# Kernel tuning notes

Measured on AMD Instinct MI355X. Metric: run time of the kernel, lower is better.

The kernel has to match this reference:

```python
import jax, jax.numpy as jnp
import numpy as np

C_IN, C = 16, 32
N = 150000
SHAPE = (480, 360, 32)
SLOPE = 0.01  # LeakyReLU default
EPS = 1e-5    # BatchNorm1d default

# offset index into the canonical 27-neighbor table, ordered (dz, dy, dx)
P133 = tuple(9 + (dy + 1) * 3 + (dx + 1) for dy in (-1, 0, 1) for dx in (-1, 0, 1))   # kernel (1,3,3)
P313 = tuple((dz + 1) * 9 + 3 + (dx + 1) for dz in (-1, 0, 1) for dx in (-1, 0, 1))   # kernel (3,1,3)
P311 = tuple((dz + 1) * 9 + 4 for dz in (-1, 0, 1))                                   # kernel (3,1,1)
P131 = tuple(9 + (dy + 1) * 3 + 1 for dy in (-1, 0, 1))                               # kernel (1,3,1)
P113 = (12, 13, 14)                                                                   # kernel (1,1,3)


def setup_inputs() -> dict:
    rng = np.random.default_rng(0)
    # unique active voxel linear coords, sorted for searchsorted lookup
    lin = np.sort(rng.choice(SHAPE[0] * SHAPE[1] * SHAPE[2], size=N, replace=False))
    z, yx = np.divmod(lin, SHAPE[1] * SHAPE[2])
    y, x = np.divmod(yx, SHAPE[2])
    coords = np.stack([z, y, x], 1)  # [N,3]
    offs = np.array([[dz, dy, dx] for dz in (-1, 0, 1) for dy in (-1, 0, 1) for dx in (-1, 0, 1)])
    nc = coords[None] + offs[:, None]  # [27,N,3]
    valid = (nc >= 0).all(-1) & (nc[..., 0] < SHAPE[0]) & (nc[..., 1] < SHAPE[1]) & (nc[..., 2] < SHAPE[2])
    nlin = nc[..., 0] * SHAPE[1] * SHAPE[2] + nc[..., 1] * SHAPE[2] + nc[..., 2]
    pos = np.clip(np.searchsorted(lin, nlin), 0, N - 1)
    found = valid & (lin[pos] == nlin)
    nbr = np.where(found, pos, -1).astype(np.int32)  # [27,N], spconv indice pairs

    key = jax.random.key(0)
    ks = jax.random.split(key, 9)
    w = lambda k, kk, ci, co: jax.random.normal(k, (kk, ci, co), jnp.float32) * (1.0 / np.sqrt(kk * ci))
    bn_params = jnp.stack([
        jnp.stack([1.0 + 0.1 * jax.random.normal(jax.random.fold_in(ks[8], 4 * i + 0), (C,)),
                   0.1 * jax.random.normal(jax.random.fold_in(ks[8], 4 * i + 1), (C,)),
                   0.1 * jax.random.normal(jax.random.fold_in(ks[8], 4 * i + 2), (C,)),
                   0.5 + jax.random.uniform(jax.random.fold_in(ks[8], 4 * i + 3), (C,))])
        for i in range(7)
    ])  # [7,4,C]: gamma, beta, running_mean, running_var
    return {
        "x_feat": jax.random.normal(ks[0], (N, C_IN), jnp.float32),
        "nbr": jnp.asarray(nbr),
        "W1": w(ks[1], 9, C_IN, C), "W12": w(ks[2], 9, C, C),
        "W2": w(ks[3], 9, C_IN, C), "W3": w(ks[4], 9, C, C),
        "Wr1": w(ks[5], 3, C, C), "Wr2": w(ks[6], 3, C, C), "Wr3": w(ks[7], 3, C, C),
        "bn_params": bn_params,
    }


def _subm(feat, nbr, W, offs):
    """Submanifold sparse conv: gather -> masked GEMM -> same active set."""
    idx = nbr[jnp.asarray(offs)]              # [K,N]
    g = feat[jnp.clip(idx, 0)]                # [K,N,Cin]
    g = jnp.where((idx >= 0)[..., None], g, jnp.zeros((), feat.dtype))
    return jnp.einsum('knc,kcd->nd', g, W)    # [N,Cout]


def _bn(f, p):  # eval-mode BatchNorm1d
    gamma, beta, mean, var = p[0], p[1], p[2], p[3]
    return gamma * (f - mean) * jax.lax.rsqrt(var + EPS) + beta


def _lrelu(f):
    return jnp.where(f >= 0, f, SLOPE * f)


def reference(x_feat, nbr, W1, W12, W2, W3, Wr1, Wr2, Wr3, bn_params):
    # ResContextBlock (downCntx): act then BN, per source
    s = _bn(_lrelu(_subm(x_feat, nbr, W1, P133)), bn_params[0])
    s = _bn(_lrelu(_subm(s, nbr, W12, P313)), bn_params[1])
    r = _bn(_lrelu(_subm(x_feat, nbr, W2, P313)), bn_params[2])
    r = _bn(_lrelu(_subm(r, nbr, W3, P133)), bn_params[3])
    y = r + s
    # ReconBlock: three axial convs -> BN -> sigmoid, summed, gating multiply
    a = jax.nn.sigmoid(_bn(_subm(y, nbr, Wr1, P311), bn_params[4]))
    b = jax.nn.sigmoid(_bn(_subm(y, nbr, Wr2, P131), bn_params[5]))
    c = jax.nn.sigmoid(_bn(_subm(y, nbr, Wr3, P113), bn_params[6]))
    return (a + b + c) * y
```

## Files before the change

### kernel.cpp

```cpp
#include <hip/hip_runtime.h>
#include <cstdint>
#include <cstddef>


#define SLOPE 0.01f
#define BN_EPS 1e-5f

typedef __attribute__((ext_vector_type(8))) short bf16x8;
typedef __attribute__((ext_vector_type(4))) float f32x4;

__device__ __forceinline__ float bflo(uint32_t w) {
    union { uint32_t i; float f; } v; v.i = w << 16; return v.f;
}
__device__ __forceinline__ float bfhi(uint32_t w) {
    union { uint32_t i; float f; } v; v.i = w & 0xffff0000u; return v.f;
}
__device__ __forceinline__ float bf2f(uint16_t u) {
    union { uint32_t i; float f; } v; v.i = ((uint32_t)u) << 16; return v.f;
}
__device__ __forceinline__ uint16_t f2bf(float f) {
    union { float f; uint32_t i; } v; v.f = f;
    uint32_t x = v.i;
    return (uint16_t)((x + 0x7fffu + ((x >> 16) & 1u)) >> 16);
}

struct Taps9 { int t[9]; };
struct WSrcs { const void* p[8]; };

#define WFS     18432
#define WF_END  (5 * WFS)
#define BN_CNT  896

__device__ __forceinline__ int detect_f32_inline(const uint16_t* x16)
{
    int lane = threadIdx.x & 63;
    float a = bf2f(x16[4 * lane]);
    float b = bf2f(x16[4 * lane + 2]);
    int bad = (!(a > -16.f && a < 16.f)) || (!(b > -16.f && b < 16.f));
    return __ballot(bad) != 0ull;
}

__device__ __forceinline__ float readw(const void* p, int j, int f32)
{
    return f32 ? ((const float*)p)[j] : bf2f(((const uint16_t*)p)[j]);
}

__global__ void prep_all(const uint16_t* __restrict__ xprobe, WSrcs srcs,
                         uint16_t* __restrict__ Wf, float* __restrict__ bnf)
{
    int f32 = detect_f32_inline(xprobe);
    int i = blockIdx.x * 256 + threadIdx.x;
    if (i < WF_END) {
        int s = i / WFS, r = i - s * WFS;
        int t = r >> 11, T = (r >> 10) & 1;
        int co = (r >> 5) & 31, k = r & 31;
        uint16_t outv;
        if (s == 0 || s == 2) {
            int c = k >> 1, p = k & 1;
            float w = readw(srcs.p[s == 0 ? 0 : 2], (t * 16 + c) * 32 + co, f32);
            uint16_t h = f2bf(w);
            outv = (T == 0) ? h : (p == 0 ? f2bf(w - bf2f(h)) : (uint16_t)0);
        } else {
            float w;
            if (s == 4) {
                int g = t / 3, kk = t - g * 3;
                const void* bnp = srcs.p[7];
                float ga = readw(bnp, (4 + g) * 128 + co, f32);
                float va = readw(bnp, (4 + g) * 128 + 96 + co, f32);
                float scl = ga * rsqrtf(va + BN_EPS);
                w = readw(srcs.p[4 + g], (kk * 32 + k) * 32 + co, f32) * scl;
            } else {
                w = readw(srcs.p[s == 1 ? 1 : 3], (t * 32 + k) * 32 + co, f32);
            }
            uint16_t h = f2bf(w);
            outv = (T == 0) ? h : f2bf(w - bf2f(h));
        }
        Wf[i] = outv;
    } else if (i < WF_END + BN_CNT) {
        bnf[i - WF_END] = readw(srcs.p[7], i - WF_END, f32);
    }
}

__global__ void canon_x3(const void* __restrict__ xsrc,
                         uint32_t* __restrict__ xi, int total)
{
    int f32 = detect_f32_inline((const uint16_t*)xsrc);
    for (int i = blockIdx.x * blockDim.x + threadIdx.x; i < total;
         i += gridDim.x * blockDim.x) {
        float v = f32 ? ((const float*)xsrc)[i]
                      : bf2f(((const uint16_t*)xsrc)[i]);
        int row = i >> 4, c = i & 15;
        uint16_t h = f2bf(v);
        uint16_t l = f2bf(v - bf2f(h));
        xi[(size_t)row * 16 + c] = (uint32_t)h | ((uint32_t)l << 16);
    }
}

struct ConvJob {
    const uint16_t* feat;
    const uint16_t* Wf;
    const float*    bn;
    const uint16_t* addsrc;
    uint16_t*       out;
    Taps9 taps;
};

#define MFMA_BF16(A, B, C) __builtin_amdgcn_mfma_f32_16x16x32_bf16(A, B, C, 0, 0, 0)

__launch_bounds__(256, 4)
__global__ void conv_mfma6(ConvJob j0, ConvJob j1,
                           const int* __restrict__ nbr, int N)
{
    const ConvJob J = (blockIdx.y == 1) ? j1 : j0;
    const int tid = threadIdx.x;
    const int n0  = blockIdx.x * 128;
    const int lane = tid & 63;
    const int m = lane & 15, q = lane >> 4;
    const int vt0 = (tid >> 6) * 32;
    const bf16x8 Z8 = {0, 0, 0, 0, 0, 0, 0, 0};

    int rows[9][2];
#pragma unroll
    for (int t = 0; t < 9; ++t)
#pragma unroll
        for (int vt = 0; vt < 2; ++vt) {
            int n = n0 + vt0 + vt * 16 + m;
            rows[t][vt] = (n < N) ? nbr[(size_t)J.taps.t[t] * N + n] : -1;
        }
    __builtin_amdgcn_sched_barrier(0);

    bool act[9][2];
#pragma unroll
    for (int t = 0; t < 9; ++t)
#pragma unroll
        for (int vt = 0; vt < 2; ++vt)
            act[t][vt] = __ballot(rows[t][vt] >= 0) != 0ull;

    f32x4 acc[2][2];
#pragma unroll
    for (int vt = 0; vt < 2; ++vt)
#pragma unroll
        for (int ot = 0; ot < 2; ++ot) acc[vt][ot] = {0.f, 0.f, 0.f, 0.f};

#pragma unroll
    for (int g = 0; g < 3; ++g) {
        bf16x8 A[3][2];
#pragma unroll
        for (int i = 0; i < 3; ++i)
#pragma unroll
            for (int vt = 0; vt < 2; ++vt) {
                const int t = g * 3 + i;
                A[i][vt] = Z8;
                if (act[t][vt]) {
                    int row = rows[t][vt];
                    if (row >= 0)
                        A[i][vt] = *(const bf16x8*)(J.feat + (size_t)row * 32 + q * 8);
                }
            }
        __builtin_amdgcn_sched_barrier(0);

#pragma unroll
        for (int i = 0; i < 3; ++i) {
            const int t = g * 3 + i;
            if (!(act[t][0] || act[t][1])) continue;
            const uint16_t* wb = J.Wf + t * 2048 + m * 32 + q * 8;
            bf16x8 B00 = *(const bf16x8*)(wb);
            bf16x8 B10 = *(const bf16x8*)(wb + 1024);
            bf16x8 B01 = *(const bf16x8*)(wb + 512);
            bf16x8 B11 = *(const bf16x8*)(wb + 1536);
#pragma unroll
            for (int vt = 0; vt < 2; ++vt) {
                if (!act[t][vt]) continue;
                acc[vt][0] = MFMA_BF16(A[i][vt], B00, acc[vt][0]);
                acc[vt][0] = MFMA_BF16(A[i][vt], B10, acc[vt][0]);
                acc[vt][1] = MFMA_BF16(A[i][vt], B01, acc[vt][1]);
                acc[vt][1] = MFMA_BF16(A[i][vt], B11, acc[vt][1]);
            }
        }
    }

#pragma unroll
    for (int ot = 0; ot < 2; ++ot) {
        int ch = ot * 16 + m;
        float ga = J.bn[ch], be = J.bn[32 + ch];
        float mu = J.bn[64 + ch], va = J.bn[96 + ch];
        float s = ga * rsqrtf(va + BN_EPS);
        float b = be - mu * s;
#pragma unroll
        for (int vt = 0; vt < 2; ++vt)
#pragma unroll
            for (int r = 0; r < 4; ++r) {
                int vox = n0 + vt0 + vt * 16 + q * 4 + r;
                if (vox >= N) continue;
                float xv = acc[vt][ot][r];
                xv = (xv >= 0.f) ? xv : SLOPE * xv;
                float o = xv * s + b;
                if (J.addsrc) o += bf2f(J.addsrc[(size_t)vox * 32 + ch]);
                J.out[(size_t)vox * 32 + ch] = f2bf(o);
            }
    }
}

__launch_bounds__(256, 4)
__global__ void recon_mfma6(const uint16_t* __restrict__ y16,
                            const uint16_t* __restrict__ xprobe,
                            const int* __restrict__ nbr,
                            const uint16_t* __restrict__ Wf4,
                            const float* __restrict__ bnf,
                            void* __restrict__ out_, int N)
{
    const int out_f32 = detect_f32_inline(xprobe);
    const int tid = threadIdx.x;
    const int n0  = blockIdx.x * 128;
    const int lane = tid & 63;
    const int m = lane & 15, q = lane >> 4;
    const int vt0 = (tid >> 6) * 32;
    const bf16x8 Z8 = {0, 0, 0, 0, 0, 0, 0, 0};

    const int ut[7] = {4, 22, 10, 16, 12, 14, 13};
    int rows[7][2];
#pragma unroll
    for (int t = 0; t < 7; ++t)
#pragma unroll
        for (int vt = 0; vt < 2; ++vt) {
            int n = n0 + vt0 + vt * 16 + m;
            rows[t][vt] = (n < N) ? nbr[(size_t)ut[t] * N + n] : -1;
        }
    __builtin_amdgcn_sched_barrier(0);

    bool act[7][2];
#pragma unroll
    for (int t = 0; t < 7; ++t)
#pragma unroll
        for (int vt = 0; vt < 2; ++vt)
            act[t][vt] = __ballot(rows[t][vt] >= 0) != 0ull;

    bf16x8 A6[2];
#pragma unroll
    for (int vt = 0; vt < 2; ++vt) {
        int row = rows[6][vt];
        A6[vt] = Z8;
        if (row >= 0)
            A6[vt] = *(const bf16x8*)(y16 + (size_t)row * 32 + q * 8);
    }

    float gsum[2][2][4];
#pragma unroll
    for (int vt = 0; vt < 2; ++vt)
#pragma unroll
        for (int ot = 0; ot < 2; ++ot)
#pragma unroll
            for (int r = 0; r < 4; ++r) gsum[vt][ot][r] = 0.f;

#pragma unroll
    for (int g = 0; g < 3; ++g) {
        f32x4 acc[2][2];
#pragma unroll
        for (int vt = 0; vt < 2; ++vt)
#pragma unroll
            for (int ot = 0; ot < 2; ++ot) acc[vt][ot] = {0.f, 0.f, 0.f, 0.f};

        bf16x8 Ae[2][2];
#pragma unroll
        for (int s2 = 0; s2 < 2; ++s2)
#pragma unroll
            for (int vt = 0; vt < 2; ++vt) {
                const int slot = 2 * g + s2;
                Ae[s2][vt] = Z8;
                if (act[slot][vt]) {
                    int row = rows[slot][vt];
                    if (row >= 0)
                        Ae[s2][vt] = *(const bf16x8*)(y16 + (size_t)row * 32 + q * 8);
                }
            }
        __builtin_amdgcn_sched_barrier(0);

#pragma unroll
        for (int s2 = 0; s2 < 2; ++s2) {
            const int slot = 2 * g + s2;
            if (!(act[slot][0] || act[slot][1])) continue;
            const int t = g * 3 + s2 * 2;
            const uint16_t* wb = Wf4 + t * 2048 + m * 32 + q * 8;
            bf16x8 B00 = *(const bf16x8*)(wb);
            bf16x8 B10 = *(const bf16x8*)(wb + 1024);
            bf16x8 B01 = *(const bf16x8*)(wb + 512);
            bf16x8 B11 = *(const bf16x8*)(wb + 1536);
#pragma unroll
            for (int vt = 0; vt < 2; ++vt) {
                if (!act[slot][vt]) continue;
                acc[vt][0] = MFMA_BF16(Ae[s2][vt], B00, acc[vt][0]);
                acc[vt][0] = MFMA_BF16(Ae[s2][vt], B10, acc[vt][0]);
                acc[vt][1] = MFMA_BF16(Ae[s2][vt], B01, acc[vt][1]);
                acc[vt][1] = MFMA_BF16(Ae[s2][vt], B11, acc[vt][1]);
            }
        }
        {
            const uint16_t* wb = Wf4 + (g * 3 + 1) * 2048 + m * 32 + q * 8;
            bf16x8 B00 = *(const bf16x8*)(wb);
            bf16x8 B10 = *(const bf16x8*)(wb + 1024);
            bf16x8 B01 = *(const bf16x8*)(wb + 512);
            bf16x8 B11 = *(const bf16x8*)(wb + 1536);
#pragma unroll
            for (int vt = 0; vt < 2; ++vt) {
                acc[vt][0] = MFMA_BF16(A6[vt], B00, acc[vt][0]);
                acc[vt][0] = MFMA_BF16(A6[vt], B10, acc[vt][0]);
                acc[vt][1] = MFMA_BF16(A6[vt], B01, acc[vt][1]);
                acc[vt][1] = MFMA_BF16(A6[vt], B11, acc[vt][1]);
            }
        }

#pragma unroll
        for (int ot = 0; ot < 2; ++ot) {
            int ch = ot * 16 + m;
            const float* p = bnf + (size_t)(4 + g) * 128;
            float scl = p[ch] * rsqrtf(p[96 + ch] + BN_EPS);
            float sh = p[32 + ch] - p[64 + ch] * scl;
#pragma unroll
            for (int vt = 0; vt < 2; ++vt)
#pragma unroll
                for (int r = 0; r < 4; ++r)
                    gsum[vt][ot][r] +=
                        1.f / (1.f + __expf(-(acc[vt][ot][r] + sh)));
        }
    }

#pragma unroll
    for (int ot = 0; ot < 2; ++ot) {
        int ch = ot * 16 + m;
#pragma unroll
        for (int vt = 0; vt < 2; ++vt)
#pragma unroll
            for (int r = 0; r < 4; ++r) {
                int vox = n0 + vt0 + vt * 16 + q * 4 + r;
                if (vox >= N) continue;
                float o = gsum[vt][ot][r] * bf2f(y16[(size_t)vox * 32 + ch]);
                if (out_f32)
                    ((float*)out_)[(size_t)vox * 32 + ch] = o;
                else
                    ((uint16_t*)out_)[(size_t)vox * 32 + ch] = f2bf(o);
            }
    }
}

#define WC_W1   0
#define WC_W12  4608
#define WC_W2   13824
#define WC_W3   18432
#define WC_WR1  27648
#define WC_WR2  30720
#define WC_WR3  33792
#define WC_BNP  36864
#define WC_END  37760

__global__ void canon_weights_fb(WSrcs srcs, float* __restrict__ Wc,
                                 const uint16_t* __restrict__ xprobe)
{
    int f32 = detect_f32_inline(xprobe);
    const int offs[9] = {WC_W1, WC_W12, WC_W2, WC_W3, WC_WR1, WC_WR2,
                         WC_WR3, WC_BNP, WC_END};
    int i = blockIdx.x * 256 + threadIdx.x;
    if (i >= WC_END) return;
    int t = 0;
#pragma unroll
    for (int k = 1; k < 8; ++k) if (i >= offs[k]) t = k;
    Wc[i] = readw(srcs.p[t], i - offs[t], f32);
}

__global__ void canon_x_bf(const void* __restrict__ xsrc,
                           uint16_t* __restrict__ xc, int n)
{
    int f32 = detect_f32_inline((const uint16_t*)xsrc);
    for (int i = blockIdx.x * blockDim.x + threadIdx.x; i < n;
         i += gridDim.x * blockDim.x) {
        float v = f32 ? ((const float*)xsrc)[i]
                      : bf2f(((const uint16_t*)xsrc)[i]);
        xc[i] = f2bf(v);
    }
}

template<int CIN>
__launch_bounds__(256)
__global__ void conv_bn_lrelu_bf(const uint16_t* __restrict__ feat,
                                 const int* __restrict__ nbr,
                                 const float* __restrict__ Wg,
                                 const float* __restrict__ bnp,
                                 const uint16_t* __restrict__ addsrc,
                                 uint16_t* __restrict__ out,
                                 Taps9 taps, int N)
{
    __shared__ float Wl[9 * CIN * 32];
    __shared__ float fs[CIN][128];
    __shared__ int   sidx[128];
    __shared__ float bns[32], bnb[32];

    const int tid = threadIdx.x;
    const int n0  = blockIdx.x * 128;

    for (int i = tid; i < 9 * CIN * 32; i += 256) Wl[i] = Wg[i];
    if (tid < 32) {
        float g = bnp[tid], b = bnp[32 + tid];
        float mu = bnp[64 + tid], va = bnp[96 + tid];
        float s = g * rsqrtf(va + BN_EPS);
        bns[tid] = s; bnb[tid] = b - mu * s;
    }
    float acc[4][4];
#pragma unroll
    for (int v = 0; v < 4; ++v)
#pragma unroll
        for (int j = 0; j < 4; ++j) acc[v][j] = 0.f;

    const int vb = (tid >> 3) << 2, cg = (tid & 7) << 2;
    const int r = tid >> 1, h = tid & 1, j0 = h * (CIN / 2);

#pragma unroll 1
    for (int t = 0; t < 9; ++t) {
        __syncthreads();
        if (tid < 128) {
            int n = n0 + tid;
            sidx[tid] = (n < N) ? nbr[(size_t)taps.t[t] * N + n] : -1;
        }
        __syncthreads();
        int mm = sidx[r];
        if (mm >= 0) {
            const uint16_t* src = feat + (size_t)mm * CIN + j0;
#pragma unroll
            for (int qq = 0; qq < CIN / 2; qq += 8) {
                uint4 u = *reinterpret_cast<const uint4*>(src + qq);
                fs[j0 + qq + 0][r] = bflo(u.x); fs[j0 + qq + 1][r] = bfhi(u.x);
                fs[j0 + qq + 2][r] = bflo(u.y); fs[j0 + qq + 3][r] = bfhi(u.y);
                fs[j0 + qq + 4][r] = bflo(u.z); fs[j0 + qq + 5][r] = bfhi(u.z);
                fs[j0 + qq + 6][r] = bflo(u.w); fs[j0 + qq + 7][r] = bfhi(u.w);
            }
        } else {
#pragma unroll
            for (int qq = 0; qq < CIN / 2; ++qq) fs[j0 + qq][r] = 0.f;
        }
        __syncthreads();
        const float* wk = Wl + t * (CIN * 32) + cg;
#pragma unroll
        for (int ci = 0; ci < CIN; ++ci) {
            float4 f = *reinterpret_cast<const float4*>(&fs[ci][vb]);
            float4 w = *reinterpret_cast<const float4*>(wk + ci * 32);
            acc[0][0] += f.x * w.x; acc[0][1] += f.x * w.y; acc[0][2] += f.x * w.z; acc[0][3] += f.x * w.w;
            acc[1][0] += f.y * w.x; acc[1][1] += f.y * w.y; acc[1][2] += f.y * w.z; acc[1][3] += f.y * w.w;
            acc[2][0] += f.z * w.x; acc[2][1] += f.z * w.y; acc[2][2] += f.z * w.z; acc[2][3] += f.z * w.w;
            acc[3][0] += f.w * w.x; acc[3][1] += f.w * w.y; acc[3][2] += f.w * w.z; acc[3][3] += f.w * w.w;
        }
    }
#pragma unroll
    for (int v = 0; v < 4; ++v) {
        int n = n0 + vb + v;
        if (n >= N) continue;
        ushort4 st;
        uint16_t* ov = (uint16_t*)&st;
#pragma unroll
        for (int j = 0; j < 4; ++j) {
            float x = acc[v][j];
            x = (x >= 0.f) ? x : SLOPE * x;
            float o = x * bns[cg + j] + bnb[cg + j];
            if (addsrc) o += bf2f(addsrc[(size_t)n * 32 + cg + j]);
            ov[j] = f2bf(o);
        }
        *reinterpret_cast<ushort4*>(out + (size_t)n * 32 + cg) = st;
    }
}

__launch_bounds__(256, 4)
__global__ void recon_gate_bf(const uint16_t* __restrict__ y,
                              const int* __restrict__ nbr,
                              const float* __restrict__ Wc,
                              const uint16_t* __restrict__ xprobe,
                              void* __restrict__ out_, int N)
{
    __shared__ float Wl[3 * 32 * 32];
    __shared__ float fs[32][128];
    __shared__ int   sidx[128];
    __shared__ float scl[3][32], shf[3][32];

    const int tid = threadIdx.x;
    const int n0  = blockIdx.x * 128;
    const int out_f32 = detect_f32_inline(xprobe);

    if (tid < 96) {
        int g = tid >> 5, c = tid & 31;
        const float* p = Wc + WC_BNP + (size_t)(4 + g) * 128;
        float ga = p[c], be = p[32 + c], mu = p[64 + c], va = p[96 + c];
        float s = ga * rsqrtf(va + BN_EPS);
        scl[g][c] = s; shf[g][c] = be - mu * s;
    }
    const int vb = (tid >> 3) << 2, cg = (tid & 7) << 2;
    const int r = tid >> 1, h = tid & 1, j0 = h * 16;

    float gsum[4][4];
#pragma unroll
    for (int v = 0; v < 4; ++v)
#pragma unroll
        for (int j = 0; j < 4; ++j) gsum[v][j] = 0.f;

    const int taps[3][3] = {{4, 13, 22}, {10, 13, 16}, {12, 13, 14}};

#pragma unroll 1
    for (int g = 0; g < 3; ++g) {
        __syncthreads();
        {
            const float* src = Wc + WC_WR1 + g * 3072;
            for (int i = tid; i < 3072; i += 256)
                Wl[i] = src[i] * scl[g][i & 31];
        }
        float acc[4][4];
#pragma unroll
        for (int v = 0; v < 4; ++v)
#pragma unroll
            for (int j = 0; j < 4; ++j) acc[v][j] = 0.f;

#pragma unroll 1
        for (int k = 0; k < 3; ++k) {
            __syncthreads();
            if (tid < 128) {
                int n = n0 + tid;
                sidx[tid] = (n < N) ? nbr[(size_t)taps[g][k] * N + n] : -1;
            }
            __syncthreads();
            int mm = sidx[r];
            if (mm >= 0) {
                const uint16_t* src = y + (size_t)mm * 32 + j0;
#pragma unroll
                for (int qq = 0; qq < 16; qq += 8) {
                    uint4 u = *reinterpret_cast<const uint4*>(src + qq);
                    fs[j0 + qq + 0][r] = bflo(u.x); fs[j0 + qq + 1][r] = bfhi(u.x);
                    fs[j0 + qq + 2][r] = bflo(u.y); fs[j0 + qq + 3][r] = bfhi(u.y);
                    fs[j0 + qq + 4][r] = bflo(u.z); fs[j0 + qq + 5][r] = bfhi(u.z);
                    fs[j0 + qq + 6][r] = bflo(u.w); fs[j0 + qq + 7][r] = bfhi(u.w);
                }
            } else {
#pragma unroll
                for (int qq = 0; qq < 16; ++qq) fs[j0 + qq][r] = 0.f;
            }
            __syncthreads();
            const float* wk = Wl + k * (32 * 32) + cg;
#pragma unroll
            for (int ci = 0; ci < 32; ++ci) {
                float4 f = *reinterpret_cast<const float4*>(&fs[ci][vb]);
                float4 w = *reinterpret_cast<const float4*>(wk + ci * 32);
                acc[0][0] += f.x * w.x; acc[0][1] += f.x * w.y; acc[0][2] += f.x * w.z; acc[0][3] += f.x * w.w;
                acc[1][0] += f.y * w.x; acc[1][1] += f.y * w.y; acc[1][2] += f.y * w.z; acc[1][3] += f.y * w.w;
                acc[2][0] += f.z * w.x; acc[2][1] += f.z * w.y; acc[2][2] += f.z * w.z; acc[2][3] += f.z * w.w;
                acc[3][0] += f.w * w.x; acc[3][1] += f.w * w.y; acc[3][2] += f.w * w.z; acc[3][3] += f.w * w.w;
            }
        }
#pragma unroll
        for (int v = 0; v < 4; ++v)
#pragma unroll
            for (int j = 0; j < 4; ++j) {
                float x = acc[v][j] + shf[g][cg + j];
                gsum[v][j] += 1.f / (1.f + __expf(-x));
            }
    }
#pragma unroll
    for (int v = 0; v < 4; ++v) {
        int n = n0 + vb + v;
        if (n >= N) continue;
#pragma unroll
        for (int j = 0; j < 4; ++j) {
            float yv = bf2f(y[(size_t)n * 32 + cg + j]);
            float o = gsum[v][j] * yv;
            if (out_f32) ((float*)out_)[(size_t)n * 32 + cg + j] = o;
            else ((uint16_t*)out_)[(size_t)n * 32 + cg + j] = f2bf(o);
        }
    }
}

extern "C" void kernel_launch(void* const* d_in, const int* in_sizes, int n_in,
                              void* d_out, int out_size, void* d_ws, size_t ws_size,
                              hipStream_t stream)
{
    (void)n_in; (void)out_size;
    const void* x   = d_in[0];
    const int*  nbr = (const int*)d_in[1];
    const int N = in_sizes[0] / 16;
    const uint16_t* xprobe = (const uint16_t*)x;

    dim3 block(256);
    const int gx = (N + 127) / 128;
    Taps9 p133 = {{9, 10, 11, 12, 13, 14, 15, 16, 17}};
    Taps9 p313 = {{3, 4, 5, 12, 13, 14, 21, 22, 23}};
    WSrcs ws8 = {{ d_in[2], d_in[3], d_in[4], d_in[5],
                   d_in[6], d_in[7], d_in[8], d_in[9] }};

    float*    bnf = (float*)d_ws;
    uint16_t* Wf  = (uint16_t*)((char*)d_ws + 4096);
    const size_t base2 = 4096u + (size_t)WF_END * 2;
    uint16_t* xi  = (uint16_t*)((char*)d_ws + base2);
    uint16_t* A1  = xi + (size_t)N * 32;
    uint16_t* A2  = A1 + (size_t)N * 32;
    uint16_t* B1  = A2 + (size_t)N * 32;
    const size_t need = base2 + 4u * (size_t)N * 64;

    if (ws_size >= need) {
        prep_all<<<(WF_END + BN_CNT + 255) / 256, block, 0, stream>>>(xprobe, ws8, Wf, bnf);
        canon_x3<<<1024, block, 0, stream>>>(x, (uint32_t*)xi, N * 16);
        ConvJob c1  = {xi, Wf + 0 * WFS, bnf + 0 * 128, nullptr, A1, p133};
        ConvJob c2  = {xi, Wf + 2 * WFS, bnf + 2 * 128, nullptr, A2, p313};
        ConvJob c12 = {A1, Wf + 1 * WFS, bnf + 1 * 128, nullptr, B1, p313};
        ConvJob c3  = {A2, Wf + 3 * WFS, bnf + 3 * 128, B1,      A1, p133};
        conv_mfma6<<<dim3(gx, 2), block, 0, stream>>>(c1, c2, nbr, N);
        conv_mfma6<<<dim3(gx, 1), block, 0, stream>>>(c12, c12, nbr, N);
        conv_mfma6<<<dim3(gx, 1), block, 0, stream>>>(c3, c3, nbr, N);
        recon_mfma6<<<gx, block, 0, stream>>>(A1, xprobe, nbr, Wf + 4 * WFS, bnf, d_out, N);
    } else {
        float*    Wc = (float*)d_ws;
        uint16_t* xc = (uint16_t*)((char*)d_ws + (size_t)WC_END * 4 + 256);
        uint16_t* A  = (uint16_t*)d_out;
        uint16_t* B  = xc + (size_t)N * 16;
        const float* bn0 = Wc + WC_BNP + 0 * 128;
        const float* bn1 = Wc + WC_BNP + 1 * 128;
        const float* bn2 = Wc + WC_BNP + 2 * 128;
        const float* bn3 = Wc + WC_BNP + 3 * 128;
        canon_weights_fb<<<(WC_END + 255) / 256, block, 0, stream>>>(ws8, Wc, xprobe);
        canon_x_bf<<<1024, block, 0, stream>>>(x, xc, N * 16);
        conv_bn_lrelu_bf<16><<<gx, block, 0, stream>>>(xc, nbr, Wc + WC_W1,  bn0, nullptr, A, p133, N);
        conv_bn_lrelu_bf<32><<<gx, block, 0, stream>>>(A,  nbr, Wc + WC_W12, bn1, nullptr, B, p313, N);
        conv_bn_lrelu_bf<16><<<gx, block, 0, stream>>>(xc, nbr, Wc + WC_W2,  bn2, nullptr, A, p313, N);
        conv_bn_lrelu_bf<32><<<gx, block, 0, stream>>>(A,  nbr, Wc + WC_W3,  bn3, B,       B, p133, N);
        recon_gate_bf<<<gx, block, 0, stream>>>(B, nbr, Wc, xprobe, d_out, N);
    }
}
```

Baseline: 170.7 us.

## Merge prep kernels, share input gathers across first convs, batch second-stage convs

Weight prep and input canonicalisation are fused into one launch. The two first-stage convs over x now run in one kernel that gathers the union of the (1,3,3) and (3,1,3) taps once and feeds two accumulator sets, so the shared taps are not fetched twice. The two second-stage convs become independent and run in a single 2-D launch: one writes bf16, the other writes fp32 residuals, and a separate add_y kernel sums them into y. This removes launches and the serial dependency between the c12 and c3 convs, at the cost of an extra fp32 buffer pass and more registers in the dual kernel.

```diff
diff --git a/kernel.cpp b/kernel.cpp
--- a/kernel.cpp
+++ b/kernel.cpp
@@ -30,6 +30,7 @@
 #define WFS     18432
 #define WF_END  (5 * WFS)
 #define BN_CNT  896
+#define PREP_BLOCKS ((WF_END + BN_CNT + 255) / 256)
 
 __device__ __forceinline__ int detect_f32_inline(const uint16_t* x16)
 {
@@ -45,54 +46,54 @@
     return f32 ? ((const float*)p)[j] : bf2f(((const uint16_t*)p)[j]);
 }
 
-__global__ void prep_all(const uint16_t* __restrict__ xprobe, WSrcs srcs,
-                         uint16_t* __restrict__ Wf, float* __restrict__ bnf)
-{
-    int f32 = detect_f32_inline(xprobe);
-    int i = blockIdx.x * 256 + threadIdx.x;
-    if (i < WF_END) {
-        int s = i / WFS, r = i - s * WFS;
-        int t = r >> 11, T = (r >> 10) & 1;
-        int co = (r >> 5) & 31, k = r & 31;
-        uint16_t outv;
-        if (s == 0 || s == 2) {
-            int c = k >> 1, p = k & 1;
-            float w = readw(srcs.p[s == 0 ? 0 : 2], (t * 16 + c) * 32 + co, f32);
-            uint16_t h = f2bf(w);
-            outv = (T == 0) ? h : (p == 0 ? f2bf(w - bf2f(h)) : (uint16_t)0);
-        } else {
-            float w;
-            if (s == 4) {
-                int g = t / 3, kk = t - g * 3;
-                const void* bnp = srcs.p[7];
-                float ga = readw(bnp, (4 + g) * 128 + co, f32);
-                float va = readw(bnp, (4 + g) * 128 + 96 + co, f32);
-                float scl = ga * rsqrtf(va + BN_EPS);
-                w = readw(srcs.p[4 + g], (kk * 32 + k) * 32 + co, f32) * scl;
+__global__ void prep_combo(const void* __restrict__ xsrc, WSrcs srcs,
+                           uint16_t* __restrict__ Wf, float* __restrict__ bnf,
+                           uint32_t* __restrict__ xi, int total)
+{
+    int f32 = detect_f32_inline((const uint16_t*)xsrc);
+    int b = blockIdx.x;
+    if (b < PREP_BLOCKS) {
+        int i = b * 256 + threadIdx.x;
+        if (i < WF_END) {
+            int s = i / WFS, r = i - s * WFS;
+            int t = r >> 11, T = (r >> 10) & 1;
+            int co = (r >> 5) & 31, k = r & 31;
+            uint16_t outv;
+            if (s == 0 || s == 2) {
+                int c = k >> 1, p = k & 1;
+                float w = readw(srcs.p[s == 0 ? 0 : 2], (t * 16 + c) * 32 + co, f32);
+                uint16_t h = f2bf(w);
+                outv = (T == 0) ? h : (p == 0 ? f2bf(w - bf2f(h)) : (uint16_t)0);
             } else {
-                w = readw(srcs.p[s == 1 ? 1 : 3], (t * 32 + k) * 32 + co, f32);
-            }
-            uint16_t h = f2bf(w);
-            outv = (T == 0) ? h : f2bf(w - bf2f(h));
-        }
-        Wf[i] = outv;
-    } else if (i < WF_END + BN_CNT) {
-        bnf[i - WF_END] = readw(srcs.p[7], i - WF_END, f32);
-    }
-}
-
-__global__ void canon_x3(const void* __restrict__ xsrc,
-                         uint32_t* __restrict__ xi, int total)
-{
-    int f32 = detect_f32_inline((const uint16_t*)xsrc);
-    for (int i = blockIdx.x * blockDim.x + threadIdx.x; i < total;
-         i += gridDim.x * blockDim.x) {
-        float v = f32 ? ((const float*)xsrc)[i]
-                      : bf2f(((const uint16_t*)xsrc)[i]);
-        int row = i >> 4, c = i & 15;
-        uint16_t h = f2bf(v);
-        uint16_t l = f2bf(v - bf2f(h));
-        xi[(size_t)row * 16 + c] = (uint32_t)h | ((uint32_t)l << 16);
+                float w;
+                if (s == 4) {
+                    int g = t / 3, kk = t - g * 3;
+                    const void* bnp = srcs.p[7];
+                    float ga = readw(bnp, (4 + g) * 128 + co, f32);
+                    float va = readw(bnp, (4 + g) * 128 + 96 + co, f32);
+                    float scl = ga * rsqrtf(va + BN_EPS);
+                    w = readw(srcs.p[4 + g], (kk * 32 + k) * 32 + co, f32) * scl;
+                } else {
+                    w = readw(srcs.p[s == 1 ? 1 : 3], (t * 32 + k) * 32 + co, f32);
+                }
+                uint16_t h = f2bf(w);
+                outv = (T == 0) ? h : f2bf(w - bf2f(h));
+            }
+            Wf[i] = outv;
+        } else if (i < WF_END + BN_CNT) {
+            bnf[i - WF_END] = readw(srcs.p[7], i - WF_END, f32);
+        }
+    } else {
+        int start = (b - PREP_BLOCKS) * 256 + threadIdx.x;
+        int stride = (gridDim.x - PREP_BLOCKS) * 256;
+        for (int i = start; i < total; i += stride) {
+            float v = f32 ? ((const float*)xsrc)[i]
+                          : bf2f(((const uint16_t*)xsrc)[i]);
+            int row = i >> 4, c = i & 15;
+            uint16_t h = f2bf(v);
+            uint16_t l = f2bf(v - bf2f(h));
+            xi[(size_t)row * 16 + c] = (uint32_t)h | ((uint32_t)l << 16);
+        }
     }
 }
 
@@ -101,14 +102,15 @@
     const uint16_t* Wf;
     const float*    bn;
     const uint16_t* addsrc;
-    uint16_t*       out;
+    void*           out;
+    int             out_fp32;
     Taps9 taps;
 };
 
 #define MFMA_BF16(A, B, C) __builtin_amdgcn_mfma_f32_16x16x32_bf16(A, B, C, 0, 0, 0)
 
 __launch_bounds__(256, 4)
-__global__ void conv_mfma6(ConvJob j0, ConvJob j1,
+__global__ void conv_mfma7(ConvJob j0, ConvJob j1,
                            const int* __restrict__ nbr, int N)
 {
     const ConvJob J = (blockIdx.y == 1) ? j1 : j0;
@@ -196,8 +198,156 @@
                 xv = (xv >= 0.f) ? xv : SLOPE * xv;
                 float o = xv * s + b;
                 if (J.addsrc) o += bf2f(J.addsrc[(size_t)vox * 32 + ch]);
-                J.out[(size_t)vox * 32 + ch] = f2bf(o);
-            }
+                if (J.out_fp32)
+                    ((float*)J.out)[(size_t)vox * 32 + ch] = o;
+                else
+                    ((uint16_t*)J.out)[(size_t)vox * 32 + ch] = f2bf(o);
+            }
+    }
+}
+
+__launch_bounds__(256, 4)
+__global__ void conv_dual(const uint16_t* __restrict__ xi,
+                          const uint16_t* __restrict__ Wf0,
+                          const uint16_t* __restrict__ Wf2,
+                          const float*    __restrict__ bnf,
+                          const int*      __restrict__ nbr,
+                          uint16_t*       __restrict__ outA,
+                          uint16_t*       __restrict__ outB,
+                          int N)
+{
+    const int tid = threadIdx.x;
+    const int n0  = blockIdx.x * 128;
+    const int lane = tid & 63;
+    const int m = lane & 15, q = lane >> 4;
+    const int vt0 = (tid >> 6) * 32;
+    const bf16x8 Z8 = {0, 0, 0, 0, 0, 0, 0, 0};
+
+    const int UT[15] = {12, 13, 14, 9, 10, 11, 15, 16, 17, 3, 4, 5, 21, 22, 23};
+    const int SB[5]  = {3, 0, 6, 0, 6};
+    const int JS[5]  = {0, 1, 1, 2, 2};
+
+    int rows[15][2];
+#pragma unroll
+    for (int u = 0; u < 15; ++u)
+#pragma unroll
+        for (int vt = 0; vt < 2; ++vt) {
+            int n = n0 + vt0 + vt * 16 + m;
+            rows[u][vt] = (n < N) ? nbr[(size_t)UT[u] * N + n] : -1;
+        }
+    __builtin_amdgcn_sched_barrier(0);
+
+    bool act[15][2];
+#pragma unroll
+    for (int u = 0; u < 15; ++u)
+#pragma unroll
+        for (int vt = 0; vt < 2; ++vt)
+            act[u][vt] = __ballot(rows[u][vt] >= 0) != 0ull;
+
+    f32x4 accA[2][2], accB[2][2];
+#pragma unroll
+    for (int vt = 0; vt < 2; ++vt)
+#pragma unroll
+        for (int ot = 0; ot < 2; ++ot) {
+            accA[vt][ot] = {0.f, 0.f, 0.f, 0.f};
+            accB[vt][ot] = {0.f, 0.f, 0.f, 0.f};
+        }
+
+#pragma unroll
+    for (int g = 0; g < 5; ++g) {
+        bf16x8 A[3][2];
+#pragma unroll
+        for (int i = 0; i < 3; ++i)
+#pragma unroll
+            for (int vt = 0; vt < 2; ++vt) {
+                const int u = g * 3 + i;
+                A[i][vt] = Z8;
+                if (act[u][vt]) {
+                    int row = rows[u][vt];
+                    if (row >= 0)
+                        A[i][vt] = *(const bf16x8*)(xi + (size_t)row * 32 + q * 8);
+                }
+            }
+        __builtin_amdgcn_sched_barrier(0);
+
+#pragma unroll
+        for (int i = 0; i < 3; ++i) {
+            const int u = g * 3 + i;
+            if (!(act[u][0] || act[u][1])) continue;
+            const int t = SB[g] + i;
+            if (JS[g] != 2) {
+                const uint16_t* wb = Wf0 + t * 2048 + m * 32 + q * 8;
+                bf16x8 B00 = *(const bf16x8*)(wb);
+                bf16x8 B10 = *(const bf16x8*)(wb + 1024);
+                bf16x8 B01 = *(const bf16x8*)(wb + 512);
+                bf16x8 B11 = *(const bf16x8*)(wb + 1536);
+#pragma unroll
+                for (int vt = 0; vt < 2; ++vt) {
+                    if (!act[u][vt]) continue;
+                    accA[vt][0] = MFMA_BF16(A[i][vt], B00, accA[vt][0]);
+                    accA[vt][0] = MFMA_BF16(A[i][vt], B10, accA[vt][0]);
+                    accA[vt][1] = MFMA_BF16(A[i][vt], B01, accA[vt][1]);
+                    accA[vt][1] = MFMA_BF16(A[i][vt], B11, accA[vt][1]);
+                }
+            }
+            if (JS[g] != 1) {
+                const uint16_t* wb = Wf2 + t * 2048 + m * 32 + q * 8;
+                bf16x8 B00 = *(const bf16x8*)(wb);
+                bf16x8 B10 = *(const bf16x8*)(wb + 1024);
+                bf16x8 B01 = *(const bf16x8*)(wb + 512);
+                bf16x8 B11 = *(const bf16x8*)(wb + 1536);
+#pragma unroll
+                for (int vt = 0; vt < 2; ++vt) {
+                    if (!act[u][vt]) continue;
+                    accB[vt][0] = MFMA_BF16(A[i][vt], B00, accB[vt][0]);
+                    accB[vt][0] = MFMA_BF16(A[i][vt], B10, accB[vt][0]);
+                    accB[vt][1] = MFMA_BF16(A[i][vt], B01, accB[vt][1]);
+                    accB[vt][1] = MFMA_BF16(A[i][vt], B11, accB[vt][1]);
+                }
+            }
+        }
+    }
+
+#pragma unroll
+    for (int jb = 0; jb < 2; ++jb) {
+        const float* bn = bnf + (jb ? 2 * 128 : 0);
+        uint16_t* out = jb ? outB : outA;
+#pragma unroll
+        for (int ot = 0; ot < 2; ++ot) {
+            int ch = ot * 16 + m;
+            float ga = bn[ch], be = bn[32 + ch];
+            float mu = bn[64 + ch], va = bn[96 + ch];
+            float s = ga * rsqrtf(va + BN_EPS);
+            float b = be - mu * s;
+#pragma unroll
+            for (int vt = 0; vt < 2; ++vt)
+#pragma unroll
+                for (int r = 0; r < 4; ++r) {
+                    int vox = n0 + vt0 + vt * 16 + q * 4 + r;
+                    if (vox >= N) continue;
+                    f32x4 av = jb ? accB[vt][ot] : accA[vt][ot];
+                    float xv = av[r];
+                    xv = (xv >= 0.f) ? xv : SLOPE * xv;
+                    out[(size_t)vox * 32 + ch] = f2bf(xv * s + b);
+                }
+        }
+    }
+}
+
+__global__ void add_y(const float* __restrict__ r32,
+                      const uint16_t* __restrict__ s16,
+                      uint16_t* __restrict__ y16, int total4)
+{
+    for (int i = blockIdx.x * blockDim.x + threadIdx.x; i < total4;
+         i += gridDim.x * blockDim.x) {
+        float4 r = ((const float4*)r32)[i];
+        ushort4 s = ((const ushort4*)s16)[i];
+        ushort4 o;
+        o.x = f2bf(r.x + bf2f(s.x));
+        o.y = f2bf(r.y + bf2f(s.y));
+        o.z = f2bf(r.z + bf2f(s.z));
+        o.w = f2bf(r.w + bf2f(s.w));
+        ((ushort4*)y16)[i] = o;
     }
 }
 
@@ -594,18 +744,18 @@
     uint16_t* A1  = xi + (size_t)N * 32;
     uint16_t* A2  = A1 + (size_t)N * 32;
     uint16_t* B1  = A2 + (size_t)N * 32;
-    const size_t need = base2 + 4u * (size_t)N * 64;
+    float*    R32 = (float*)(B1 + (size_t)N * 32);
+    const size_t need = base2 + 4u * (size_t)N * 64 + (size_t)N * 128;
 
     if (ws_size >= need) {
-        prep_all<<<(WF_END + BN_CNT + 255) / 256, block, 0, stream>>>(xprobe, ws8, Wf, bnf);
-        canon_x3<<<1024, block, 0, stream>>>(x, (uint32_t*)xi, N * 16);
-        ConvJob c1  = {xi, Wf + 0 * WFS, bnf + 0 * 128, nullptr, A1, p133};
-        ConvJob c2  = {xi, Wf + 2 * WFS, bnf + 2 * 128, nullptr, A2, p313};
-        ConvJob c12 = {A1, Wf + 1 * WFS, bnf + 1 * 128, nullptr, B1, p313};
-        ConvJob c3  = {A2, Wf + 3 * WFS, bnf + 3 * 128, B1,      A1, p133};
-        conv_mfma6<<<dim3(gx, 2), block, 0, stream>>>(c1, c2, nbr, N);
-        conv_mfma6<<<dim3(gx, 1), block, 0, stream>>>(c12, c12, nbr, N);
-        conv_mfma6<<<dim3(gx, 1), block, 0, stream>>>(c3, c3, nbr, N);
+        prep_combo<<<PREP_BLOCKS + 1024, block, 0, stream>>>(
+            x, ws8, Wf, bnf, (uint32_t*)xi, N * 16);
+        conv_dual<<<gx, block, 0, stream>>>(xi, Wf + 0 * WFS, Wf + 2 * WFS,
+                                            bnf, nbr, A1, A2, N);
+        ConvJob c12 = {A1, Wf + 1 * WFS, bnf + 1 * 128, nullptr, B1,  0, p313};
+        ConvJob c3  = {A2, Wf + 3 * WFS, bnf + 3 * 128, nullptr, R32, 1, p133};
+        conv_mfma7<<<dim3(gx, 2), block, 0, stream>>>(c12, c3, nbr, N);
+        add_y<<<1024, block, 0, stream>>>(R32, B1, A1, N * 8);
         recon_mfma6<<<gx, block, 0, stream>>>(A1, xprobe, nbr, Wf + 4 * WFS, bnf, d_out, N);
     } else {
         float*    Wc = (float*)d_ws;
```

Result: no change. 174.1 us (+2.0%).
